# Optimization experiments

Measured on AMD Instinct MI355X. Metric: run time of the kernel, lower is better.

The kernel has to match this reference:

```python
import jax, jax.numpy as jnp
import numpy as np


def _mlp(x, w1, b1, w2, b2):
    # torch Mlp: fc1 -> GELU (exact erf) -> fc2, dropout off in eval
    h = jax.nn.gelu(x @ w1 + b1, approximate=False)
    return h @ w2 + b2


def _nearest(x, oh, ow):
    # torch F.interpolate mode='nearest' on [B,h,w,d]: src = floor(dst*in/out)
    h, w = x.shape[1], x.shape[2]
    ih = (np.arange(oh) * h) // oh
    iw = (np.arange(ow) * w) // ow
    return x[:, ih][:, :, iw]


def setup_inputs() -> dict:
    key = jax.random.key(0)
    ks = jax.random.split(key, 8)
    B, s0, dim, nPnt, new2 = 4, 12, 256, 128, 48  # new_size=24
    sc = 0.02
    return {
        "token_init": jax.random.normal(ks[0], (B, s0, s0, dim), jnp.float32),
        "point_token": jax.random.normal(ks[1], (B, nPnt, dim), jnp.float32),
        "nr_w1": jax.random.normal(ks[2], (nPnt, 4 * nPnt), jnp.float32) * sc,
        "nr_b1": jnp.zeros((4 * nPnt,), jnp.float32),
        "nr_w2": jax.random.normal(ks[3], (4 * nPnt, nPnt), jnp.float32) * sc,
        "nr_b2": jnp.zeros((nPnt,), jnp.float32),
        "na_w1": jax.random.normal(ks[4], (nPnt, 4 * nPnt), jnp.float32) * sc,
        "na_b1": jnp.zeros((4 * nPnt,), jnp.float32),
        "na_w2": jax.random.normal(ks[5], (4 * nPnt, nPnt), jnp.float32) * sc,
        "na_b2": jnp.zeros((nPnt,), jnp.float32),
        "tf_w1": jax.random.normal(ks[6], (new2, new2), jnp.float32) * sc,
        "tf_b1": jnp.zeros((new2,), jnp.float32),
        "tf_w2": jax.random.normal(ks[7], (new2, 1), jnp.float32) * sc,
        "tf_b2": jnp.zeros((1,), jnp.float32),
        "height": 120,
        "width": 160,
    }


def reference(token_init, point_token, nr_w1, nr_b1, nr_w2, nr_b2,
              na_w1, na_b1, na_w2, na_b2, tf_w1, tf_b1, tf_w2, tf_b2,
              height, width):
    B, nPnt, dim = point_token.shape
    new_size = tf_w1.shape[0] // 2
    scale = dim ** (-0.5)
    # is_init=False path: repeat_interleave x2 along H and W
    t = jnp.repeat(jnp.repeat(token_init, 2, axis=1), 2, axis=2)  # [B,2s,2s,d]
    token_raw = _nearest(t, height, width)                        # [B,H,W,d]
    t_exp = _nearest(t, new_size, new_size)                       # [B,sH,sW,d]
    sH = sW = new_size
    token_templ = t_exp.reshape(B, sH * sW, dim)
    node_adj = jnp.einsum('bnd,bpd->bnp', token_templ, point_token) * scale
    node_adj = _mlp(node_adj, nr_w1, nr_b1, nr_w2, nr_b2)
    node_adj = node_adj.reshape(B, sH, sW, nPnt)
    node_w = jnp.einsum('bhwp,bhwd->bhpd', node_adj, t_exp) * (sW ** -0.5)
    node_h = jnp.einsum('bhwp,bhwd->bwpd', node_adj, t_exp) * (sH ** -0.5)
    token_n = jnp.concatenate([node_w, node_h], axis=1)           # [B,2s,nPnt,d]
    x = token_n.reshape(B, sH + sW, nPnt * dim).transpose(0, 2, 1)  # [B,nPnt*d,2s]
    token_fused = _mlp(x, tf_w1, tf_b1, tf_w2, tf_b2)             # [B,nPnt*d,1]
    token_fused = token_fused.reshape(B, nPnt, dim)
    token_raw_f = token_raw.reshape(B, height * width, dim)
    node_attn = jnp.einsum('bnd,bpd->bnp', token_raw_f, point_token) * scale
    node_attn = jax.nn.softmax(_mlp(node_attn, na_w1, na_b1, na_w2, na_b2), axis=-1)
    token_new = node_attn @ token_fused + token_raw_f             # [B,HW,d]
    return token_new
```

## Files before the change

### kernel.cpp

```cpp
#include <hip/hip_runtime.h>
#include <math.h>

#define B     4
#define DIM   256
#define NP    128
#define NS    144
#define HID   512
#define NROW  576
#define H_OUT 120
#define W_OUT 160

__device__ __forceinline__ float gelu_exact(float x) {
    return 0.5f * x * (1.0f + erff(x * 0.70710678118654752440f));
}

__global__ __launch_bounds__(256) void k_t(
    const float* __restrict__ pt, float* __restrict__ ptT)
{
    const int bid = blockIdx.x;
    const int b   = bid >> 5;
    const int rem = bid & 31;
    const int d0  = (rem >> 2) * 32;
    const int p0  = (rem & 3) * 32;
    const int t   = threadIdx.x;
    __shared__ float tile[32][33];

    #pragma unroll
    for (int i = t; i < 1024; i += 256) {
        const int row = i >> 5, col = i & 31;
        tile[row][col] = pt[(size_t)(b * NP + p0 + row) * DIM + d0 + col];
    }
    __syncthreads();
    #pragma unroll
    for (int i = t; i < 1024; i += 256) {
        const int row = i >> 5, col = i & 31;
        ptT[(size_t)(b * DIM + d0 + row) * NP + p0 + col] = tile[col][row];
    }
}

__global__ __launch_bounds__(256) void k_mlp(
    const float* __restrict__ ti, const float* __restrict__ ptT,
    const float* __restrict__ nr_w1, const float* __restrict__ nr_b1,
    const float* __restrict__ nr_w2, const float* __restrict__ nr_b2,
    const float* __restrict__ na_w1, const float* __restrict__ na_b1,
    const float* __restrict__ na_w2, const float* __restrict__ na_b2,
    float* __restrict__ nadjT, float* __restrict__ attn)
{
    const int mlp  = blockIdx.x / 144;
    const int tile = blockIdx.x % 144;
    const int g0 = tile * 4;
    const int b  = g0 / NS;
    const int n0 = g0 % NS;
    const int t  = threadIdx.x;

    const float* __restrict__ w1 = mlp ? na_w1 : nr_w1;
    const float* __restrict__ b1 = mlp ? na_b1 : nr_b1;
    const float* __restrict__ w2 = mlp ? na_w2 : nr_w2;
    const float* __restrict__ b2 = mlp ? na_b2 : nr_b2;

    __shared__ float xs[4][DIM];
    __shared__ float parA[2][4][NP];
    __shared__ float qs[4][NP];
    __shared__ float hs[4][HID];
    __shared__ float par[8][4][NP];
    __shared__ float red[4][NP];

    {
        const int r = t >> 6, c = t & 63;
        ((float4*)xs[r])[c] = ((const float4*)ti)[(size_t)(g0 + r) * 64 + c];
    }
    __syncthreads();

    {
        const int pq = t & 31;
        const int rr = (t >> 5) & 3;
        const int dh = t >> 7;
        const float4* __restrict__ pT4 =
            (const float4*)(ptT + (size_t)b * DIM * NP) + pq;
        float4 acc = make_float4(0.f, 0.f, 0.f, 0.f);
        #pragma unroll 8
        for (int d2 = 0; d2 < 128; ++d2) {
            const int d = dh * 128 + d2;
            const float4 v4 = pT4[(size_t)d * 32];
            const float  xv = xs[rr][d];
            acc.x += xv * v4.x; acc.y += xv * v4.y;
            acc.z += xv * v4.z; acc.w += xv * v4.w;
        }
        ((float4*)parA[dh][rr])[pq] = acc;
    }
    __syncthreads();

    const int p  = t & 127;
    const int rh = t >> 7;
    qs[rh][p]     = (parA[0][rh][p]     + parA[1][rh][p])     * 0.0625f;
    qs[rh + 2][p] = (parA[0][rh + 2][p] + parA[1][rh + 2][p]) * 0.0625f;
    __syncthreads();

    {
        const int kq = t & 127;
        const int k0 = kq * 4;
        float4 acc0 = *(const float4*)(b1 + k0);
        float4 acc1 = acc0;
        const float* __restrict__ wp = w1 + k0;
        #pragma unroll 8
        for (int pp = 0; pp < NP; ++pp) {
            const float4 w4 = *(const float4*)(wp + (size_t)pp * HID);
            const float q0 = qs[rh][pp];
            const float q1 = qs[rh + 2][pp];
            acc0.x += q0*w4.x; acc0.y += q0*w4.y;
            acc0.z += q0*w4.z; acc0.w += q0*w4.w;
            acc1.x += q1*w4.x; acc1.y += q1*w4.y;
            acc1.z += q1*w4.z; acc1.w += q1*w4.w;
        }
        float4 o0, o1;
        o0.x = gelu_exact(acc0.x); o0.y = gelu_exact(acc0.y);
        o0.z = gelu_exact(acc0.z); o0.w = gelu_exact(acc0.w);
        o1.x = gelu_exact(acc1.x); o1.y = gelu_exact(acc1.y);
        o1.z = gelu_exact(acc1.z); o1.w = gelu_exact(acc1.w);
        ((float4*)hs[rh])[kq]     = o0;
        ((float4*)hs[rh + 2])[kq] = o1;
    }
    __syncthreads();

    {
        const int pq = t & 31;
        const int p0 = pq * 4;
        const int kg = t >> 5;
        float4 a0 = make_float4(0.f,0.f,0.f,0.f);
        float4 a1 = a0, a2 = a0, a3 = a0;
        const float4* __restrict__ w24 = (const float4*)(w2 + p0);
        #pragma unroll 8
        for (int i = 0; i < 64; ++i) {
            const int k = kg * 64 + i;
            const float4 w4 = w24[(size_t)k * 32];
            const float h0 = hs[0][k], h1 = hs[1][k];
            const float h2 = hs[2][k], h3 = hs[3][k];
            a0.x += h0*w4.x; a0.y += h0*w4.y; a0.z += h0*w4.z; a0.w += h0*w4.w;
            a1.x += h1*w4.x; a1.y += h1*w4.y; a1.z += h1*w4.z; a1.w += h1*w4.w;
            a2.x += h2*w4.x; a2.y += h2*w4.y; a2.z += h2*w4.z; a2.w += h2*w4.w;
            a3.x += h3*w4.x; a3.y += h3*w4.y; a3.z += h3*w4.z; a3.w += h3*w4.w;
        }
        ((float4*)par[kg][0])[pq] = a0;
        ((float4*)par[kg][1])[pq] = a1;
        ((float4*)par[kg][2])[pq] = a2;
        ((float4*)par[kg][3])[pq] = a3;
    }
    __syncthreads();

    float lg0 = b2[p], lg1 = lg0;
    #pragma unroll
    for (int kg = 0; kg < 8; ++kg) {
        lg0 += par[kg][rh][p];
        lg1 += par[kg][rh + 2][p];
    }

    if (mlp == 0) {
        float* __restrict__ dst = nadjT + (size_t)(b * NP + p) * NS + n0;
        dst[rh]     = lg0;
        dst[rh + 2] = lg1;
    } else {
        red[rh][p] = lg0; red[rh + 2][p] = lg1;
        __syncthreads();
        for (int s = 64; s > 0; s >>= 1) {
            if (p < s) {
                red[rh][p]     = fmaxf(red[rh][p],     red[rh][p + s]);
                red[rh + 2][p] = fmaxf(red[rh + 2][p], red[rh + 2][p + s]);
            }
            __syncthreads();
        }
        const float m0 = red[rh][0], m1 = red[rh + 2][0];
        __syncthreads();
        const float e0 = expf(lg0 - m0), e1 = expf(lg1 - m1);
        red[rh][p] = e0; red[rh + 2][p] = e1;
        __syncthreads();
        for (int s = 64; s > 0; s >>= 1) {
            if (p < s) {
                red[rh][p]     += red[rh][p + s];
                red[rh + 2][p] += red[rh + 2][p + s];
            }
            __syncthreads();
        }
        attn[(size_t)(g0 + rh) * NP + p]     = e0 / red[rh][0];
        attn[(size_t)(g0 + rh + 2) * NP + p] = e1 / red[rh + 2][0];
    }
}

__global__ __launch_bounds__(256) void k_fold(
    const float* __restrict__ nadjT, const float* __restrict__ ti,
    const float* __restrict__ w1, const float* __restrict__ b1,
    const float* __restrict__ w2, const float* __restrict__ b2,
    float* __restrict__ tf)
{
    const int b = blockIdx.x >> 7;
    const int p = blockIdx.x & 127;
    const int t = threadIdx.x;
    __shared__ float an[NS];
    __shared__ float w1p[24][48];
    __shared__ float b1s[48];
    __shared__ float w2s[48];

    if (t < 36) {
        ((float4*)an)[t] =
            ((const float4*)(nadjT + (size_t)(b * NP + p) * NS))[t];
    }
    if (t >= 192 && t < 240) {
        const int k = t - 192;
        b1s[k] = b1[k];
        w2s[k] = w2[k];
    }
    for (int i = t; i < 24 * 48; i += 256) {
        const int m = i / 48, k = i - m * 48;
        w1p[m][k] = w1[(2 * m) * 48 + k] + w1[(2 * m + 1) * 48 + k];
    }
    __syncthreads();

    const int d = t;
    const float* __restrict__ tb = ti + (size_t)b * NS * DIM + d;
    float v[24];
    #pragma unroll
    for (int m = 0; m < 24; ++m) v[m] = 0.f;
    #pragma unroll
    for (int y = 0; y < 12; ++y) {
        #pragma unroll
        for (int x = 0; x < 12; ++x) {
            const int n = y * 12 + x;
            const float tv = tb[n * DIM];
            const float a  = an[n];
            v[y]      += a * tv;
            v[12 + x] += a * tv;
        }
    }
    const float c = 0.40824829046386301637f;
    #pragma unroll
    for (int m = 0; m < 24; ++m) v[m] *= c;

    float acc = b2[0];
    for (int k = 0; k < 48; ++k) {
        float tt = b1s[k];
        #pragma unroll
        for (int m = 0; m < 24; ++m) tt += v[m] * w1p[m][k];
        acc += gelu_exact(tt) * w2s[k];
    }
    tf[(size_t)(b * NP + p) * DIM + d] = acc;
}

__global__ __launch_bounds__(256) void k_final(
    const float* __restrict__ attn, const float* __restrict__ tf,
    const float* __restrict__ ti, float4* __restrict__ out)
{
    const int g    = blockIdx.x >> 1;
    const int half = blockIdx.x & 1;
    const int b = g / NS;
    const int n = g % NS;
    const int t = threadIdx.x;
    const int dq = t & 63;
    const int pg = t >> 6;

    __shared__ float  at[NP];
    __shared__ float4 par4[4][64];
    __shared__ float4 rowf[64];

    if (t < NP) at[t] = attn[(size_t)g * NP + t];
    __syncthreads();

    const float4* __restrict__ tp = (const float4*)tf + (size_t)b * NP * 64 + dq;
    float4 acc = make_float4(0.f, 0.f, 0.f, 0.f);
    #pragma unroll 8
    for (int i = 0; i < 32; ++i) {
        const int pp = pg * 32 + i;
        const float  a  = at[pp];
        const float4 tv = tp[(size_t)pp * 64];
        acc.x += a * tv.x; acc.y += a * tv.y;
        acc.z += a * tv.z; acc.w += a * tv.w;
    }
    par4[pg][dq] = acc;
    __syncthreads();

    if (t < 64) {
        float4 s = par4[0][t];
        const float4 s1 = par4[1][t], s2 = par4[2][t], s3 = par4[3][t];
        const float4 tiv = ((const float4*)ti)[(size_t)g * 64 + t];
        s.x += s1.x + s2.x + s3.x + tiv.x;
        s.y += s1.y + s2.y + s3.y + tiv.y;
        s.z += s1.z + s2.z + s3.z + tiv.z;
        s.w += s1.w + s2.w + s3.w + tiv.w;
        rowf[t] = s;
    }
    __syncthreads();

    const int y = n / 12, x = n % 12;
    const int w_lo = (40 * x + 2) / 3;
    const int w_hi = (40 * x + 42) / 3;
    const float4 val = rowf[dq];
    const int h0 = 10 * y + 5 * half;
    for (int h = h0; h < h0 + 5; ++h) {
        float4* __restrict__ orow = out + (size_t)((b * H_OUT + h) * W_OUT) * 64 + dq;
        for (int w = w_lo + pg; w < w_hi; w += 4) {
            orow[(size_t)w * 64] = val;
        }
    }
}

extern "C" void kernel_launch(void* const* d_in, const int* in_sizes, int n_in,
                              void* d_out, int out_size, void* d_ws, size_t ws_size,
                              hipStream_t stream) {
    (void)in_sizes; (void)n_in; (void)out_size; (void)ws_size;
    const float* token_init  = (const float*)d_in[0];
    const float* point_token = (const float*)d_in[1];
    const float* nr_w1 = (const float*)d_in[2];
    const float* nr_b1 = (const float*)d_in[3];
    const float* nr_w2 = (const float*)d_in[4];
    const float* nr_b2 = (const float*)d_in[5];
    const float* na_w1 = (const float*)d_in[6];
    const float* na_b1 = (const float*)d_in[7];
    const float* na_w2 = (const float*)d_in[8];
    const float* na_b2 = (const float*)d_in[9];
    const float* tf_w1 = (const float*)d_in[10];
    const float* tf_b1 = (const float*)d_in[11];
    const float* tf_w2 = (const float*)d_in[12];
    const float* tf_b2 = (const float*)d_in[13];

    float* out = (float*)d_out;
    float* ws  = (float*)d_ws;
    float* nadjT = ws;
    float* attn  = nadjT + NROW * NP;
    float* tf    = attn + NROW * NP;
    float* ptT   = tf + B * NP * DIM;

    k_t<<<128, 256, 0, stream>>>(point_token, ptT);
    k_mlp<<<288, 256, 0, stream>>>(token_init, ptT,
                                   nr_w1, nr_b1, nr_w2, nr_b2,
                                   na_w1, na_b1, na_w2, na_b2,
                                   nadjT, attn);
    k_fold<<<B * NP, 256, 0, stream>>>(nadjT, token_init,
                                       tf_w1, tf_b1, tf_w2, tf_b2, tf);
    k_final<<<NROW * 2, 256, 0, stream>>>(attn, tf, token_init, (float4*)out);
}
```

Before: 170.3 us.

## Fuse four kernels into one cooperative persistent kernel with grid syncs

Replaces the transpose, MLP, fold and final kernel launches with a single cooperative kernel of 256 blocks that runs each stage in turn and separates them with grid.sync(). This removes the per-launch overhead and the gaps between dependent kernels. In exchange each stage now runs on only 256 blocks instead of up to 1152, so the MLP, fold and final stages loop over extra tasks, which may lower parallelism. The original four-kernel launch sequence is kept as a fallback if the cooperative launch fails.

```diff
diff --git a/kernel.cpp b/kernel.cpp
--- a/kernel.cpp
+++ b/kernel.cpp
@@ -1,5 +1,8 @@
 #include <hip/hip_runtime.h>
+#include <hip/hip_cooperative_groups.h>
 #include <math.h>
+
+namespace cg = cooperative_groups;
 
 #define B     4
 #define DIM   256
@@ -12,6 +15,314 @@
 
 __device__ __forceinline__ float gelu_exact(float x) {
     return 0.5f * x * (1.0f + erff(x * 0.70710678118654752440f));
+}
+
+struct SmMlp {
+    float xs[4][DIM];
+    float parA[2][4][NP];
+    float qs[4][NP];
+    float hs[4][HID];
+    float par[8][4][NP];
+    float red[4][NP];
+};
+struct SmFold {
+    float an[NS];
+    float w1p[24][48];
+    float b1s[48];
+    float w2s[48];
+};
+struct SmFin {
+    float  at[NP];
+    float4 par4[4][64];
+    float4 rowf[64];
+};
+
+__global__ __launch_bounds__(256, 2) void k_all(
+    const float* __restrict__ ti, const float* __restrict__ pt,
+    const float* __restrict__ nr_w1, const float* __restrict__ nr_b1,
+    const float* __restrict__ nr_w2, const float* __restrict__ nr_b2,
+    const float* __restrict__ na_w1, const float* __restrict__ na_b1,
+    const float* __restrict__ na_w2, const float* __restrict__ na_b2,
+    const float* __restrict__ tf_w1, const float* __restrict__ tf_b1,
+    const float* __restrict__ tf_w2, const float* __restrict__ tf_b2,
+    float* __restrict__ nadjT, float* __restrict__ attn,
+    float* __restrict__ tfb, float* __restrict__ ptT,
+    float4* __restrict__ out)
+{
+    cg::grid_group grid = cg::this_grid();
+    const int blk = blockIdx.x;
+    const int t   = threadIdx.x;
+
+    __shared__ __align__(16) char smraw[sizeof(SmMlp)];
+
+    if (blk < 128) {
+        float (*tile)[33] = reinterpret_cast<float (*)[33]>(smraw);
+        const int b   = blk >> 5;
+        const int rem = blk & 31;
+        const int d0  = (rem >> 2) * 32;
+        const int p0  = (rem & 3) * 32;
+        #pragma unroll
+        for (int i = t; i < 1024; i += 256) {
+            const int row = i >> 5, col = i & 31;
+            tile[row][col] = pt[(size_t)(b * NP + p0 + row) * DIM + d0 + col];
+        }
+        __syncthreads();
+        #pragma unroll
+        for (int i = t; i < 1024; i += 256) {
+            const int row = i >> 5, col = i & 31;
+            ptT[(size_t)(b * DIM + d0 + row) * NP + p0 + col] = tile[col][row];
+        }
+    }
+    __threadfence();
+    grid.sync();
+    __threadfence();
+
+    {
+        SmMlp& s = *reinterpret_cast<SmMlp*>(smraw);
+        for (int task = blk; task < 288; task += 256) {
+            __syncthreads();
+            const int mlp  = task / 144;
+            const int tile = task % 144;
+            const int g0 = tile * 4;
+            const int b  = g0 / NS;
+            const int n0 = g0 % NS;
+
+            const float* __restrict__ w1 = mlp ? na_w1 : nr_w1;
+            const float* __restrict__ b1 = mlp ? na_b1 : nr_b1;
+            const float* __restrict__ w2 = mlp ? na_w2 : nr_w2;
+            const float* __restrict__ b2 = mlp ? na_b2 : nr_b2;
+
+            {
+                const int r = t >> 6, c = t & 63;
+                ((float4*)s.xs[r])[c] =
+                    ((const float4*)ti)[(size_t)(g0 + r) * 64 + c];
+            }
+            __syncthreads();
+            {
+                const int pq = t & 31;
+                const int rr = (t >> 5) & 3;
+                const int dh = t >> 7;
+                const float4* __restrict__ pT4 =
+                    (const float4*)(ptT + (size_t)b * DIM * NP) + pq;
+                float4 acc = make_float4(0.f, 0.f, 0.f, 0.f);
+                #pragma unroll 8
+                for (int d2 = 0; d2 < 128; ++d2) {
+                    const int d = dh * 128 + d2;
+                    const float4 v4 = pT4[(size_t)d * 32];
+                    const float  xv = s.xs[rr][d];
+                    acc.x += xv * v4.x; acc.y += xv * v4.y;
+                    acc.z += xv * v4.z; acc.w += xv * v4.w;
+                }
+                ((float4*)s.parA[dh][rr])[pq] = acc;
+            }
+            __syncthreads();
+
+            const int p  = t & 127;
+            const int rh = t >> 7;
+            s.qs[rh][p]     = (s.parA[0][rh][p]     + s.parA[1][rh][p])     * 0.0625f;
+            s.qs[rh + 2][p] = (s.parA[0][rh + 2][p] + s.parA[1][rh + 2][p]) * 0.0625f;
+            __syncthreads();
+
+            {
+                const int kq = t & 127;
+                const int k0 = kq * 4;
+                float4 acc0 = *(const float4*)(b1 + k0);
+                float4 acc1 = acc0;
+                const float* __restrict__ wp = w1 + k0;
+                #pragma unroll 8
+                for (int pp = 0; pp < NP; ++pp) {
+                    const float4 w4 = *(const float4*)(wp + (size_t)pp * HID);
+                    const float q0 = s.qs[rh][pp];
+                    const float q1 = s.qs[rh + 2][pp];
+                    acc0.x += q0*w4.x; acc0.y += q0*w4.y;
+                    acc0.z += q0*w4.z; acc0.w += q0*w4.w;
+                    acc1.x += q1*w4.x; acc1.y += q1*w4.y;
+                    acc1.z += q1*w4.z; acc1.w += q1*w4.w;
+                }
+                float4 o0, o1;
+                o0.x = gelu_exact(acc0.x); o0.y = gelu_exact(acc0.y);
+                o0.z = gelu_exact(acc0.z); o0.w = gelu_exact(acc0.w);
+                o1.x = gelu_exact(acc1.x); o1.y = gelu_exact(acc1.y);
+                o1.z = gelu_exact(acc1.z); o1.w = gelu_exact(acc1.w);
+                ((float4*)s.hs[rh])[kq]     = o0;
+                ((float4*)s.hs[rh + 2])[kq] = o1;
+            }
+            __syncthreads();
+
+            {
+                const int pq = t & 31;
+                const int p0 = pq * 4;
+                const int kg = t >> 5;
+                float4 a0 = make_float4(0.f,0.f,0.f,0.f);
+                float4 a1 = a0, a2 = a0, a3 = a0;
+                const float4* __restrict__ w24 = (const float4*)(w2 + p0);
+                #pragma unroll 8
+                for (int i = 0; i < 64; ++i) {
+                    const int k = kg * 64 + i;
+                    const float4 w4 = w24[(size_t)k * 32];
+                    const float h0 = s.hs[0][k], h1 = s.hs[1][k];
+                    const float h2 = s.hs[2][k], h3 = s.hs[3][k];
+                    a0.x += h0*w4.x; a0.y += h0*w4.y; a0.z += h0*w4.z; a0.w += h0*w4.w;
+                    a1.x += h1*w4.x; a1.y += h1*w4.y; a1.z += h1*w4.z; a1.w += h1*w4.w;
+                    a2.x += h2*w4.x; a2.y += h2*w4.y; a2.z += h2*w4.z; a2.w += h2*w4.w;
+                    a3.x += h3*w4.x; a3.y += h3*w4.y; a3.z += h3*w4.z; a3.w += h3*w4.w;
+                }
+                ((float4*)s.par[kg][0])[pq] = a0;
+                ((float4*)s.par[kg][1])[pq] = a1;
+                ((float4*)s.par[kg][2])[pq] = a2;
+                ((float4*)s.par[kg][3])[pq] = a3;
+            }
+            __syncthreads();
+
+            float lg0 = b2[p], lg1 = lg0;
+            #pragma unroll
+            for (int kg = 0; kg < 8; ++kg) {
+                lg0 += s.par[kg][rh][p];
+                lg1 += s.par[kg][rh + 2][p];
+            }
+
+            if (mlp == 0) {
+                float* __restrict__ dst = nadjT + (size_t)(b * NP + p) * NS + n0;
+                dst[rh]     = lg0;
+                dst[rh + 2] = lg1;
+            } else {
+                s.red[rh][p] = lg0; s.red[rh + 2][p] = lg1;
+                __syncthreads();
+                for (int sw = 64; sw > 0; sw >>= 1) {
+                    if (p < sw) {
+                        s.red[rh][p]     = fmaxf(s.red[rh][p],     s.red[rh][p + sw]);
+                        s.red[rh + 2][p] = fmaxf(s.red[rh + 2][p], s.red[rh + 2][p + sw]);
+                    }
+                    __syncthreads();
+                }
+                const float m0 = s.red[rh][0], m1 = s.red[rh + 2][0];
+                __syncthreads();
+                const float e0 = expf(lg0 - m0), e1 = expf(lg1 - m1);
+                s.red[rh][p] = e0; s.red[rh + 2][p] = e1;
+                __syncthreads();
+                for (int sw = 64; sw > 0; sw >>= 1) {
+                    if (p < sw) {
+                        s.red[rh][p]     += s.red[rh][p + sw];
+                        s.red[rh + 2][p] += s.red[rh + 2][p + sw];
+                    }
+                    __syncthreads();
+                }
+                attn[(size_t)(g0 + rh) * NP + p]     = e0 / s.red[rh][0];
+                attn[(size_t)(g0 + rh + 2) * NP + p] = e1 / s.red[rh + 2][0];
+            }
+        }
+    }
+    __threadfence();
+    grid.sync();
+    __threadfence();
+
+    {
+        SmFold& s = *reinterpret_cast<SmFold*>(smraw);
+        if (t >= 192 && t < 240) {
+            const int k = t - 192;
+            s.b1s[k] = tf_b1[k];
+            s.w2s[k] = tf_w2[k];
+        }
+        for (int i = t; i < 24 * 48; i += 256) {
+            const int m = i / 48, k = i - m * 48;
+            s.w1p[m][k] = tf_w1[(2 * m) * 48 + k] + tf_w1[(2 * m + 1) * 48 + k];
+        }
+        for (int task = blk; task < 512; task += 256) {
+            __syncthreads();
+            const int b = task >> 7;
+            const int p = task & 127;
+            if (t < 36) {
+                ((float4*)s.an)[t] =
+                    ((const float4*)(nadjT + (size_t)(b * NP + p) * NS))[t];
+            }
+            __syncthreads();
+
+            const int d = t;
+            const float* __restrict__ tb = ti + (size_t)b * NS * DIM + d;
+            float v[24];
+            #pragma unroll
+            for (int m = 0; m < 24; ++m) v[m] = 0.f;
+            #pragma unroll
+            for (int y = 0; y < 12; ++y) {
+                #pragma unroll
+                for (int x = 0; x < 12; ++x) {
+                    const int n = y * 12 + x;
+                    const float tv = tb[n * DIM];
+                    const float a  = s.an[n];
+                    v[y]      += a * tv;
+                    v[12 + x] += a * tv;
+                }
+            }
+            const float c = 0.40824829046386301637f;
+            #pragma unroll
+            for (int m = 0; m < 24; ++m) v[m] *= c;
+
+            float acc = tf_b2[0];
+            for (int k = 0; k < 48; ++k) {
+                float tt = s.b1s[k];
+                #pragma unroll
+                for (int m = 0; m < 24; ++m) tt += v[m] * s.w1p[m][k];
+                acc += gelu_exact(tt) * s.w2s[k];
+            }
+            tfb[(size_t)(b * NP + p) * DIM + d] = acc;
+        }
+    }
+    __threadfence();
+    grid.sync();
+    __threadfence();
+
+    {
+        SmFin& s = *reinterpret_cast<SmFin*>(smraw);
+        const int dq = t & 63;
+        const int pg = t >> 6;
+        for (int g = blk; g < NROW; g += 256) {
+            __syncthreads();
+            const int b = g / NS;
+            const int n = g % NS;
+
+            if (t < NP) s.at[t] = attn[(size_t)g * NP + t];
+            __syncthreads();
+
+            const float4* __restrict__ tp =
+                (const float4*)tfb + (size_t)b * NP * 64 + dq;
+            float4 acc = make_float4(0.f, 0.f, 0.f, 0.f);
+            #pragma unroll 8
+            for (int i = 0; i < 32; ++i) {
+                const int pp = pg * 32 + i;
+                const float  a  = s.at[pp];
+                const float4 tv = tp[(size_t)pp * 64];
+                acc.x += a * tv.x; acc.y += a * tv.y;
+                acc.z += a * tv.z; acc.w += a * tv.w;
+            }
+            s.par4[pg][dq] = acc;
+            __syncthreads();
+
+            if (t < 64) {
+                float4 sv = s.par4[0][t];
+                const float4 s1 = s.par4[1][t], s2 = s.par4[2][t], s3 = s.par4[3][t];
+                const float4 tiv = ((const float4*)ti)[(size_t)g * 64 + t];
+                sv.x += s1.x + s2.x + s3.x + tiv.x;
+                sv.y += s1.y + s2.y + s3.y + tiv.y;
+                sv.z += s1.z + s2.z + s3.z + tiv.z;
+                sv.w += s1.w + s2.w + s3.w + tiv.w;
+                s.rowf[t] = sv;
+            }
+            __syncthreads();
+
+            const int y = n / 12, x = n % 12;
+            const int w_lo = (40 * x + 2) / 3;
+            const int w_hi = (40 * x + 42) / 3;
+            const float4 val = s.rowf[dq];
+            const int h0 = 10 * y;
+            for (int h = h0; h < h0 + 10; ++h) {
+                float4* __restrict__ orow =
+                    out + (size_t)((b * H_OUT + h) * W_OUT) * 64 + dq;
+                for (int w = w_lo + pg; w < w_hi; w += 4) {
+                    orow[(size_t)w * 64] = val;
+                }
+            }
+        }
+    }
 }
 
 __global__ __launch_bounds__(256) void k_t(
@@ -320,19 +631,31 @@
     const float* tf_w2 = (const float*)d_in[12];
     const float* tf_b2 = (const float*)d_in[13];
 
-    float* out = (float*)d_out;
     float* ws  = (float*)d_ws;
     float* nadjT = ws;
     float* attn  = nadjT + NROW * NP;
-    float* tf    = attn + NROW * NP;
-    float* ptT   = tf + B * NP * DIM;
-
-    k_t<<<128, 256, 0, stream>>>(point_token, ptT);
-    k_mlp<<<288, 256, 0, stream>>>(token_init, ptT,
-                                   nr_w1, nr_b1, nr_w2, nr_b2,
-                                   na_w1, na_b1, na_w2, na_b2,
-                                   nadjT, attn);
-    k_fold<<<B * NP, 256, 0, stream>>>(nadjT, token_init,
-                                       tf_w1, tf_b1, tf_w2, tf_b2, tf);
-    k_final<<<NROW * 2, 256, 0, stream>>>(attn, tf, token_init, (float4*)out);
+    float* tfb   = attn + NROW * NP;
+    float* ptT   = tfb + B * NP * DIM;
+    float4* out4 = (float4*)d_out;
+
+    void* args[] = {
+        (void*)&token_init, (void*)&point_token,
+        (void*)&nr_w1, (void*)&nr_b1, (void*)&nr_w2, (void*)&nr_b2,
+        (void*)&na_w1, (void*)&na_b1, (void*)&na_w2, (void*)&na_b2,
+        (void*)&tf_w1, (void*)&tf_b1, (void*)&tf_w2, (void*)&tf_b2,
+        (void*)&nadjT, (void*)&attn, (void*)&tfb, (void*)&ptT, (void*)&out4
+    };
+    hipError_t err = hipLaunchCooperativeKernel((const void*)k_all, dim3(256),
+                                                dim3(256), args, 0, stream);
+    if (err != hipSuccess) {
+        (void)hipGetLastError();
+        k_t<<<128, 256, 0, stream>>>(point_token, ptT);
+        k_mlp<<<288, 256, 0, stream>>>(token_init, ptT,
+                                       nr_w1, nr_b1, nr_w2, nr_b2,
+                                       na_w1, na_b1, na_w2, na_b2,
+                                       nadjT, attn);
+        k_fold<<<B * NP, 256, 0, stream>>>(nadjT, token_init,
+                                           tf_w1, tf_b1, tf_w2, tf_b2, tfb);
+        k_final<<<NROW * 2, 256, 0, stream>>>(attn, tfb, token_init, out4);
+    }
 }
```

Result: slower. 426.5 us (+150.5%).
